# Kernel optimization log

Measured on AMD Instinct MI355X. Metric: run time of the kernel, lower is better.

Reference implementation:

```python
import jax, jax.numpy as jnp
import numpy as np

NUM_SENT, SENT_LEN, HIDDEN, OUT = 128, 64, 512, 512
N = NUM_SENT * SENT_LEN


def setup_inputs() -> dict:
    key = jax.random.key(0)
    ks = jax.random.split(key, 14)
    s = 1.0 / np.sqrt(HIDDEN)
    so = 1.0 / np.sqrt(OUT)
    return {
        "x": jax.random.normal(ks[0], (NUM_SENT, SENT_LEN, HIDDEN), jnp.float32),
        "mask": jax.random.uniform(ks[1], (N,), jnp.float32),
        "a_ud": jax.random.normal(ks[2], (N, N), jnp.float32) * 0.01,
        "a_lr": jax.random.normal(ks[3], (N, N), jnp.float32) * 0.01,
        "W": jax.random.uniform(ks[4], (OUT, HIDDEN), jnp.float32, -s, s),
        "b": jax.random.uniform(ks[5], (OUT,), jnp.float32, -s, s),
        "W_ud": jax.random.uniform(ks[6], (OUT, HIDDEN), jnp.float32, -s, s),
        "b_ud": jax.random.uniform(ks[7], (OUT,), jnp.float32, -s, s),
        "W_lr": jax.random.uniform(ks[8], (OUT, HIDDEN), jnp.float32, -s, s),
        "b_lr": jax.random.uniform(ks[9], (OUT,), jnp.float32, -s, s),
        "W_g": jax.random.uniform(ks[10], (OUT, HIDDEN), jnp.float32, -s, s),
        "b_g": jax.random.uniform(ks[11], (OUT,), jnp.float32, -s, s),
        "W_go": jax.random.uniform(ks[12], (OUT, OUT), jnp.float32, -so, so),
        "b_go": jax.random.uniform(ks[13], (OUT,), jnp.float32, -so, so),
    }


def reference(x, mask, a_ud, a_lr, W, b, W_ud, b_ud, W_lr, b_lr, W_g, b_g, W_go, b_go):
    num_sent, sent_len, hidden = x.shape
    xf = x.reshape(-1, hidden)                       # [N, H]
    h_ud = a_ud @ xf                                 # [N, H] neighbor aggregation (up/down)
    h_lr = a_lr @ xf                                 # [N, H] neighbor aggregation (left/right)
    h = (xf @ W.T + b) + (h_ud @ W_ud.T + b_ud) + (h_lr @ W_lr.T + b_lr)  # [N, OUT]
    # global node branch: masked mean-pool of relu(linear_g(x))
    n = mask.sum()
    h_g = (mask[None, :] @ jax.nn.relu(xf @ W_g.T + b_g)) / n  # [1, OUT]
    h = h + (h_g @ W_go.T + b_go)                    # broadcast add over N rows
    h = jax.nn.relu(h).reshape(num_sent, sent_len, -1)
    return (h, h_g)
```

## Files before the change

kernel.cpp:

```cpp
#include <hip/hip_runtime.h>
#include <stdint.h>


typedef __attribute__((ext_vector_type(8))) short short8;
typedef __attribute__((ext_vector_type(4))) float f32x4;

typedef const __attribute__((address_space(1))) void* gas1_t;
typedef __attribute__((address_space(3))) void* las3_t;

__device__ __forceinline__ void gload16(const void* g, void* l) {
  __builtin_amdgcn_global_load_lds((gas1_t)g, (las3_t)l, 16, 0, 0);
}

__device__ __forceinline__ unsigned pack2t(float lo, float hi) {
  return __builtin_amdgcn_perm(__float_as_uint(hi), __float_as_uint(lo), 0x07060302u);
}

__device__ __forceinline__ unsigned f2bf_rne(float f) {
  unsigned u = __float_as_uint(f);
  return (u + 0x7FFFu + ((u >> 16) & 1u)) >> 16;
}
__device__ __forceinline__ unsigned pack2_rne(float lo, float hi) {
  return f2bf_rne(lo) | (f2bf_rne(hi) << 16);
}

__global__ __launch_bounds__(256) void k1_convert(
    const float* __restrict__ x, const float* __restrict__ W,
    const float* __restrict__ W_ud, const float* __restrict__ W_lr,
    const float* __restrict__ W_g,
    uint16_t* __restrict__ xb, uint16_t* __restrict__ Yt, uint16_t* __restrict__ Wb1)
{
  unsigned tid = blockIdx.x * 256u + threadIdx.x;
  const float* src;
  uint16_t* dst;
  if (tid < 524288u) {
    src = x + (size_t)tid * 8;
    dst = xb + (size_t)tid * 8;
  } else {
    unsigned r = tid - 524288u;
    unsigned which = r >> 15;
    unsigned e8 = (r & 32767u) * 8;
    src = (which == 0 ? W : which == 1 ? W_ud : which == 2 ? W_lr : W_g) + e8;
    if (which == 0) {
      unsigned n = e8 >> 9, k = e8 & 511u;
      dst = Yt + (size_t)n * 16896 + 16384 + k;
    } else {
      dst = Wb1 + (size_t)(which - 1) * 262144 + e8;
    }
  }
  float4 v0 = ((const float4*)src)[0];
  float4 v1 = ((const float4*)src)[1];
  uint4 p;
  p.x = pack2_rne(v0.x, v0.y); p.y = pack2_rne(v0.z, v0.w);
  p.z = pack2_rne(v1.x, v1.y); p.w = pack2_rne(v1.z, v1.w);
  *(uint4*)dst = p;
}

__global__ __launch_bounds__(256) void k2_gemm1(
    const uint16_t* __restrict__ xb, const uint16_t* __restrict__ Wb1,
    const float* __restrict__ mask, const float* __restrict__ b_g,
    uint16_t* __restrict__ Yt, float* __restrict__ tg)
{
  __shared__ __align__(16) char smem[34816];
  char* const bufA = smem;
  char* const bufB = smem + 8192;

  const int t = threadIdx.x;
  const int i0 = blockIdx.x * 128;
  const int bn = blockIdx.y;
  const int n0 = bn * 128;
  const int lane = t & 63, w = t >> 6;
  const int q = lane >> 4, l15 = lane & 15;
  const int wm = w >> 1, wn = w & 1;
  const int srow = t >> 2, spart = t & 3;

  f32x4 acc[4][4] = {};

  const uint16_t* const aA0 = xb + (size_t)(i0 + srow) * 512 + spart * 8;
  const uint16_t* const aA1 = aA0 + (size_t)64 * 512;
  const uint16_t* const aB0 = Wb1 + (size_t)(n0 + srow) * 512 + spart * 8;
  const uint16_t* const aB1 = aB0 + (size_t)64 * 512;

  for (int s = 0; s < 16; ++s) {
    __syncthreads();
    const int kk = s << 5;
    gload16(aA0 + kk, bufA + t * 16);
    gload16(aA1 + kk, bufA + 4096 + t * 16);
    gload16(aB0 + kk, bufB + t * 16);
    gload16(aB1 + kk, bufB + 4096 + t * 16);
    __syncthreads();
    short8 af[4], bf[4];
#pragma unroll
    for (int mi = 0; mi < 4; ++mi)
      af[mi] = *(const short8*)(bufA + (wm * 64 + mi * 16 + l15) * 64 + q * 16);
#pragma unroll
    for (int ni = 0; ni < 4; ++ni)
      bf[ni] = *(const short8*)(bufB + (wn * 64 + ni * 16 + l15) * 64 + q * 16);
#pragma unroll
    for (int mi = 0; mi < 4; ++mi)
#pragma unroll
      for (int ni = 0; ni < 4; ++ni)
        acc[mi][ni] = __builtin_amdgcn_mfma_f32_16x16x32_bf16(af[mi], bf[ni], acc[mi][ni], 0, 0, 0);
  }
  __syncthreads();

  const int g = bn >> 2;
  const int jb = (bn & 3) * 128;

  if (g < 2) {
    uint16_t* T = (uint16_t*)smem;
#pragma unroll
    for (int mi = 0; mi < 4; ++mi) {
#pragma unroll
      for (int ni = 0; ni < 4; ++ni) {
        int jl = wn * 64 + ni * 16 + l15;
#pragma unroll
        for (int r = 0; r < 4; ++r) {
          int il = wm * 64 + mi * 16 + q * 4 + r;
          T[jl * 136 + il] = (uint16_t)f2bf_rne(acc[mi][ni][r]);
        }
      }
    }
    __syncthreads();
    const int jl = t >> 1, half = t & 1;
    uint16_t* dst = Yt + (size_t)(jb + jl) * 16896 + (size_t)g * 8192 + i0 + half * 64;
    const uint16_t* srcT = T + jl * 136 + half * 64;
#pragma unroll
    for (int c = 0; c < 8; ++c)
      *(uint4*)(dst + c * 8) = *(const uint4*)(srcT + c * 8);
  } else {
#pragma unroll
    for (int mi = 0; mi < 4; ++mi) {
#pragma unroll
      for (int ni = 0; ni < 4; ++ni) {
        int jl = jb + wn * 64 + ni * 16 + l15;
        float bg = b_g[jl];
#pragma unroll
        for (int r = 0; r < 4; ++r) {
          int il = i0 + wm * 64 + mi * 16 + q * 4 + r;
          float v = fmaxf(acc[mi][ni][r] + bg, 0.f) * mask[il];
          tg[(size_t)il * 512 + jl] = v;
        }
      }
    }
  }
}

__global__ __launch_bounds__(256) void k3_reduce(const float* __restrict__ tg,
                                                 float* __restrict__ colsum)
{
  const int t = threadIdx.x;
  const int r0 = blockIdx.x * 64;
  float a0 = 0.f, a1 = 0.f;
  for (int r = 0; r < 64; ++r) {
    const float* row = tg + (size_t)(r0 + r) * 512;
    a0 += row[t];
    a1 += row[t + 256];
  }
  atomicAdd(&colsum[t], a0);
  atomicAdd(&colsum[t + 256], a1);
}

__global__ __launch_bounds__(256) void k4_finalize(
    const float* __restrict__ colsum, const float* __restrict__ mask,
    const float* __restrict__ b, const float* __restrict__ b_ud,
    const float* __restrict__ b_lr, const float* __restrict__ W_go,
    const float* __restrict__ b_go,
    float* __restrict__ row_add, float* __restrict__ out_hg)
{
  __shared__ float red[256];
  __shared__ float hg[512];
  const int t = threadIdx.x;
  float s = 0.f;
  for (int k = t; k < 8192; k += 256) s += mask[k];
  red[t] = s;
  __syncthreads();
  for (int o = 128; o > 0; o >>= 1) {
    if (t < o) red[t] += red[t + o];
    __syncthreads();
  }
  const float n = red[0];
  for (int j = t; j < 512; j += 256) hg[j] = colsum[j] / n;
  __syncthreads();

  const int j0 = blockIdx.x * 64;
  const int jj = j0 + (t >> 2);
  const int seg = t & 3;
  const float4* wrow = (const float4*)(W_go + (size_t)jj * 512 + seg * 128);
  float p = 0.f;
#pragma unroll 4
  for (int c = 0; c < 32; ++c) {
    float4 wv = wrow[c];
    const float* h4 = &hg[seg * 128 + c * 4];
    p += wv.x * h4[0] + wv.y * h4[1] + wv.z * h4[2] + wv.w * h4[3];
  }
  p += __shfl_down(p, 2);
  p += __shfl_down(p, 1);
  if ((t & 3) == 0)
    row_add[jj] = b[jj] + b_ud[jj] + b_lr[jj] + b_go[jj] + p;
  if (t < 64) out_hg[j0 + t] = hg[j0 + t];
}

__global__ __launch_bounds__(256) void k5_gemm_big(
    const float* __restrict__ a_ud, const float* __restrict__ a_lr,
    const float* __restrict__ x, const uint16_t* __restrict__ Yt,
    const float* __restrict__ row_add, float* __restrict__ out)
{
  __shared__ __align__(16) char smem[26624];
  char* const bufA0 = smem;
  char* const bufA1 = smem + 5120;
  char* const bufB0 = smem + 10240;
  char* const bufB1 = smem + 18432;

  const int t = threadIdx.x;
  const int i0 = blockIdx.x * 64;
  const int j0 = blockIdx.y * 128;
  const int lane = t & 63, w = t >> 6;
  const int q = lane >> 4, l15 = lane & 15;
  const int wm = w >> 1, wn = w & 1;
  const int srow = t >> 2, spart = t & 3;

  f32x4 acc[2][4] = {};

  const size_t aoff_big = (size_t)(i0 + srow) * 8192 + spart * 8;
  const size_t aoff_x   = (size_t)(i0 + srow) * 512 + spart * 8;
  const uint16_t* const bsrc0 = Yt + (size_t)(j0 + srow) * 16896 + spart * 8;
  const uint16_t* const bsrc1 = bsrc0 + (size_t)64 * 16896;
  const int aw = srow * 80 + spart * 16;

  float4 pA0, pA1;

  {
    const float* asrc = a_ud + aoff_big;
    pA0 = ((const float4*)asrc)[0];
    pA1 = ((const float4*)asrc)[1];
    gload16(bsrc0, bufB0 + t * 16);
    gload16(bsrc1, bufB0 + 4096 + t * 16);
    uint4 pk;
    pk.x = pack2t(pA0.x, pA0.y); pk.y = pack2t(pA0.z, pA0.w);
    pk.z = pack2t(pA1.x, pA1.y); pk.w = pack2t(pA1.z, pA1.w);
    *(uint4*)(bufA0 + aw) = pk;
  }

  for (int s = 0; s < 528; ++s) {
    __syncthreads();
    const int nxt = s + 1;
    const bool more = (nxt < 528);
    char* const cA = (s & 1) ? bufA1 : bufA0;
    char* const cB = (s & 1) ? bufB1 : bufB0;
    char* const nA = (s & 1) ? bufA0 : bufA1;
    char* const nB = (s & 1) ? bufB0 : bufB1;

    if (more) {
      const float* asrc;
      if (nxt < 256)      asrc = a_ud + aoff_big + (nxt << 5);
      else if (nxt < 512) asrc = a_lr + aoff_big + ((nxt - 256) << 5);
      else                asrc = x + aoff_x + ((nxt - 512) << 5);
      pA0 = ((const float4*)asrc)[0];
      pA1 = ((const float4*)asrc)[1];
      const int bk = nxt << 5;
      gload16(bsrc0 + bk, nB + t * 16);
      gload16(bsrc1 + bk, nB + 4096 + t * 16);
    }

    short8 af0 = *(const short8*)(cA + (wm * 32 + l15) * 80 + q * 16);
    short8 af1 = *(const short8*)(cA + (wm * 32 + 16 + l15) * 80 + q * 16);
    short8 bf0 = *(const short8*)(cB + (wn * 64 + l15) * 64 + q * 16);
    short8 bf1 = *(const short8*)(cB + (wn * 64 + 16 + l15) * 64 + q * 16);
    short8 bf2 = *(const short8*)(cB + (wn * 64 + 32 + l15) * 64 + q * 16);
    short8 bf3 = *(const short8*)(cB + (wn * 64 + 48 + l15) * 64 + q * 16);

    acc[0][0] = __builtin_amdgcn_mfma_f32_16x16x32_bf16(af0, bf0, acc[0][0], 0, 0, 0);
    acc[0][1] = __builtin_amdgcn_mfma_f32_16x16x32_bf16(af0, bf1, acc[0][1], 0, 0, 0);
    acc[0][2] = __builtin_amdgcn_mfma_f32_16x16x32_bf16(af0, bf2, acc[0][2], 0, 0, 0);
    acc[0][3] = __builtin_amdgcn_mfma_f32_16x16x32_bf16(af0, bf3, acc[0][3], 0, 0, 0);
    acc[1][0] = __builtin_amdgcn_mfma_f32_16x16x32_bf16(af1, bf0, acc[1][0], 0, 0, 0);
    acc[1][1] = __builtin_amdgcn_mfma_f32_16x16x32_bf16(af1, bf1, acc[1][1], 0, 0, 0);
    acc[1][2] = __builtin_amdgcn_mfma_f32_16x16x32_bf16(af1, bf2, acc[1][2], 0, 0, 0);
    acc[1][3] = __builtin_amdgcn_mfma_f32_16x16x32_bf16(af1, bf3, acc[1][3], 0, 0, 0);

    if (more) {
      uint4 pk;
      pk.x = pack2t(pA0.x, pA0.y); pk.y = pack2t(pA0.z, pA0.w);
      pk.z = pack2t(pA1.x, pA1.y); pk.w = pack2t(pA1.z, pA1.w);
      *(uint4*)(nA + aw) = pk;
    }
  }

#pragma unroll
  for (int ni = 0; ni < 4; ++ni) {
    const int jl = j0 + wn * 64 + ni * 16 + l15;
    const float ra = row_add[jl];
#pragma unroll
    for (int mi = 0; mi < 2; ++mi) {
#pragma unroll
      for (int r = 0; r < 4; ++r) {
        const int il = i0 + wm * 32 + mi * 16 + q * 4 + r;
        out[(size_t)il * 512 + jl] = fmaxf(acc[mi][ni][r] + ra, 0.f);
      }
    }
  }
}

extern "C" void kernel_launch(void* const* d_in, const int* in_sizes, int n_in,
                              void* d_out, int out_size, void* d_ws, size_t ws_size,
                              hipStream_t stream) {
  (void)in_sizes; (void)n_in; (void)out_size; (void)ws_size;
  const float* x    = (const float*)d_in[0];
  const float* mask = (const float*)d_in[1];
  const float* a_ud = (const float*)d_in[2];
  const float* a_lr = (const float*)d_in[3];
  const float* W    = (const float*)d_in[4];
  const float* b    = (const float*)d_in[5];
  const float* W_ud = (const float*)d_in[6];
  const float* b_ud = (const float*)d_in[7];
  const float* W_lr = (const float*)d_in[8];
  const float* b_lr = (const float*)d_in[9];
  const float* W_g  = (const float*)d_in[10];
  const float* b_g  = (const float*)d_in[11];
  const float* W_go = (const float*)d_in[12];
  const float* b_go = (const float*)d_in[13];
  float* out = (float*)d_out;

  char* ws = (char*)d_ws;
  uint16_t* xb     = (uint16_t*)(ws);
  uint16_t* Yt     = (uint16_t*)(ws + 8388608);
  uint16_t* Wb1    = (uint16_t*)(ws + 25690112);
  float*    tg     = (float*)(ws + 27262976);
  float*    colsum = (float*)(ws + 44040192);
  float*    rowadd = (float*)(ws + 44042240);

  hipMemsetAsync(colsum, 0, 512 * sizeof(float), stream);
  k1_convert<<<2560, 256, 0, stream>>>(x, W, W_ud, W_lr, W_g, xb, Yt, Wb1);
  k2_gemm1<<<dim3(64, 12), 256, 0, stream>>>(xb, Wb1, mask, b_g, Yt, tg);
  k3_reduce<<<128, 256, 0, stream>>>(tg, colsum);
  k4_finalize<<<8, 256, 0, stream>>>(colsum, mask, b, b_ud, b_lr, W_go, b_go,
                                     rowadd, out + 4194304);
  k5_gemm_big<<<dim3(128, 4), 256, 0, stream>>>(a_ud, a_lr, x, Yt, rowadd, out);
}
```

Baseline: 1.006 ms.

## Split-K the big GEMM, widen K tile with swizzled LDS, fuse global-pool reduction

The large GEMM now splits its K dimension (a_ud|a_lr|x, 16896) into two halves across blockIdx.z. That doubles the grid from 512 to 1024 blocks to fill more CUs. It also uses a 64-wide K step with an XOR-swizzled B layout in LDS to cut bank conflicts and halve the barrier count. A new combine kernel adds the partial sums, the row bias and applies ReLU, which costs an extra pass over the 16 MB output. The masked relu column sum is folded into the first GEMM epilogue with shuffles and atomics, removing the tg intermediate and the separate reduce kernel.

```diff
diff --git a/kernel.cpp b/kernel.cpp
--- a/kernel.cpp
+++ b/kernel.cpp
@@ -59,7 +59,7 @@
 __global__ __launch_bounds__(256) void k2_gemm1(
     const uint16_t* __restrict__ xb, const uint16_t* __restrict__ Wb1,
     const float* __restrict__ mask, const float* __restrict__ b_g,
-    uint16_t* __restrict__ Yt, float* __restrict__ tg)
+    uint16_t* __restrict__ Yt, float* __restrict__ colsum)
 {
   __shared__ __align__(16) char smem[34816];
   char* const bufA = smem;
@@ -129,36 +129,27 @@
     for (int c = 0; c < 8; ++c)
       *(uint4*)(dst + c * 8) = *(const uint4*)(srcT + c * 8);
   } else {
-#pragma unroll
-    for (int mi = 0; mi < 4; ++mi) {
-#pragma unroll
-      for (int ni = 0; ni < 4; ++ni) {
-        int jl = jb + wn * 64 + ni * 16 + l15;
-        float bg = b_g[jl];
-#pragma unroll
-        for (int r = 0; r < 4; ++r) {
-          int il = i0 + wm * 64 + mi * 16 + q * 4 + r;
-          float v = fmaxf(acc[mi][ni][r] + bg, 0.f) * mask[il];
-          tg[(size_t)il * 512 + jl] = v;
-        }
-      }
-    }
-  }
-}
-
-__global__ __launch_bounds__(256) void k3_reduce(const float* __restrict__ tg,
-                                                 float* __restrict__ colsum)
-{
-  const int t = threadIdx.x;
-  const int r0 = blockIdx.x * 64;
-  float a0 = 0.f, a1 = 0.f;
-  for (int r = 0; r < 64; ++r) {
-    const float* row = tg + (size_t)(r0 + r) * 512;
-    a0 += row[t];
-    a1 += row[t + 256];
-  }
-  atomicAdd(&colsum[t], a0);
-  atomicAdd(&colsum[t + 256], a1);
+    float mk[4][4];
+#pragma unroll
+    for (int mi = 0; mi < 4; ++mi)
+#pragma unroll
+      for (int r = 0; r < 4; ++r)
+        mk[mi][r] = mask[i0 + wm * 64 + mi * 16 + q * 4 + r];
+#pragma unroll
+    for (int ni = 0; ni < 4; ++ni) {
+      const int jl = jb + wn * 64 + ni * 16 + l15;
+      const float bg = b_g[jl];
+      float p = 0.f;
+#pragma unroll
+      for (int mi = 0; mi < 4; ++mi)
+#pragma unroll
+        for (int r = 0; r < 4; ++r)
+          p += fmaxf(acc[mi][ni][r] + bg, 0.f) * mk[mi][r];
+      p += __shfl_xor(p, 16);
+      p += __shfl_xor(p, 32);
+      if (q == 0) atomicAdd(&colsum[jl], p);
+    }
+  }
 }
 
 __global__ __launch_bounds__(256) void k4_finalize(
@@ -204,102 +195,136 @@
 __global__ __launch_bounds__(256) void k5_gemm_big(
     const float* __restrict__ a_ud, const float* __restrict__ a_lr,
     const float* __restrict__ x, const uint16_t* __restrict__ Yt,
-    const float* __restrict__ row_add, float* __restrict__ out)
-{
-  __shared__ __align__(16) char smem[26624];
-  char* const bufA0 = smem;
-  char* const bufA1 = smem + 5120;
-  char* const bufB0 = smem + 10240;
-  char* const bufB1 = smem + 18432;
+    float* __restrict__ out, float* __restrict__ P1)
+{
+  __shared__ __align__(16) char smem[51200];
+  char* const A0 = smem;
+  char* const A1 = smem + 9216;
+  char* const B0 = smem + 18432;
+  char* const B1 = smem + 34816;
 
   const int t = threadIdx.x;
   const int i0 = blockIdx.x * 64;
   const int j0 = blockIdx.y * 128;
-  const int lane = t & 63, w = t >> 6;
+  const int z  = blockIdx.z;
+  const int lane = t & 63;
   const int q = lane >> 4, l15 = lane & 15;
+  const int w = t >> 6;
   const int wm = w >> 1, wn = w & 1;
-  const int srow = t >> 2, spart = t & 3;
+
+  const int arow = t >> 2, aseg = t & 3;
+  const int brow = t >> 3;
+  const int bchunk = (t & 7) ^ ((t >> 3) & 7);
 
   f32x4 acc[2][4] = {};
-
-  const size_t aoff_big = (size_t)(i0 + srow) * 8192 + spart * 8;
-  const size_t aoff_x   = (size_t)(i0 + srow) * 512 + spart * 8;
-  const uint16_t* const bsrc0 = Yt + (size_t)(j0 + srow) * 16896 + spart * 8;
-  const uint16_t* const bsrc1 = bsrc0 + (size_t)64 * 16896;
-  const int aw = srow * 80 + spart * 16;
-
-  float4 pA0, pA1;
+  const int kbase0 = z * 8448;
+
+  float4 av0, av1, av2, av3;
+#define A_SRC(gk) ((gk) < 8192 \
+    ? a_ud + (size_t)(i0 + arow) * 8192 + (gk) + aseg * 16 \
+    : ((gk) < 16384 \
+      ? a_lr + (size_t)(i0 + arow) * 8192 + ((gk) - 8192) + aseg * 16 \
+      : x + (size_t)(i0 + arow) * 512 + ((gk) - 16384) + aseg * 16))
 
   {
-    const float* asrc = a_ud + aoff_big;
-    pA0 = ((const float4*)asrc)[0];
-    pA1 = ((const float4*)asrc)[1];
-    gload16(bsrc0, bufB0 + t * 16);
-    gload16(bsrc1, bufB0 + 4096 + t * 16);
-    uint4 pk;
-    pk.x = pack2t(pA0.x, pA0.y); pk.y = pack2t(pA0.z, pA0.w);
-    pk.z = pack2t(pA1.x, pA1.y); pk.w = pack2t(pA1.z, pA1.w);
-    *(uint4*)(bufA0 + aw) = pk;
-  }
-
-  for (int s = 0; s < 528; ++s) {
-    __syncthreads();
-    const int nxt = s + 1;
-    const bool more = (nxt < 528);
-    char* const cA = (s & 1) ? bufA1 : bufA0;
-    char* const cB = (s & 1) ? bufB1 : bufB0;
-    char* const nA = (s & 1) ? bufA0 : bufA1;
-    char* const nB = (s & 1) ? bufB0 : bufB1;
+    const float* as = A_SRC(kbase0);
+    av0 = ((const float4*)as)[0]; av1 = ((const float4*)as)[1];
+    av2 = ((const float4*)as)[2]; av3 = ((const float4*)as)[3];
+#pragma unroll
+    for (int r = 0; r < 4; ++r) {
+      const int jrow = r * 32 + brow;
+      gload16(Yt + (size_t)(j0 + jrow) * 16896 + kbase0 + bchunk * 8,
+              B0 + r * 4096 + t * 16);
+    }
+    uint4 p0, p1;
+    p0.x = pack2t(av0.x, av0.y); p0.y = pack2t(av0.z, av0.w);
+    p0.z = pack2t(av1.x, av1.y); p0.w = pack2t(av1.z, av1.w);
+    p1.x = pack2t(av2.x, av2.y); p1.y = pack2t(av2.z, av2.w);
+    p1.z = pack2t(av3.x, av3.y); p1.w = pack2t(av3.z, av3.w);
+    *(uint4*)(A0 + arow * 144 + aseg * 32) = p0;
+    *(uint4*)(A0 + arow * 144 + aseg * 32 + 16) = p1;
+  }
+
+  for (int s = 0; s < 132; ++s) {
+    __syncthreads();
+    const bool more = (s + 1 < 132);
+    char* const cA = (s & 1) ? A1 : A0;
+    char* const cB = (s & 1) ? B1 : B0;
+    char* const nA = (s & 1) ? A0 : A1;
+    char* const nB = (s & 1) ? B0 : B1;
 
     if (more) {
-      const float* asrc;
-      if (nxt < 256)      asrc = a_ud + aoff_big + (nxt << 5);
-      else if (nxt < 512) asrc = a_lr + aoff_big + ((nxt - 256) << 5);
-      else                asrc = x + aoff_x + ((nxt - 512) << 5);
-      pA0 = ((const float4*)asrc)[0];
-      pA1 = ((const float4*)asrc)[1];
-      const int bk = nxt << 5;
-      gload16(bsrc0 + bk, nB + t * 16);
-      gload16(bsrc1 + bk, nB + 4096 + t * 16);
-    }
-
-    short8 af0 = *(const short8*)(cA + (wm * 32 + l15) * 80 + q * 16);
-    short8 af1 = *(const short8*)(cA + (wm * 32 + 16 + l15) * 80 + q * 16);
-    short8 bf0 = *(const short8*)(cB + (wn * 64 + l15) * 64 + q * 16);
-    short8 bf1 = *(const short8*)(cB + (wn * 64 + 16 + l15) * 64 + q * 16);
-    short8 bf2 = *(const short8*)(cB + (wn * 64 + 32 + l15) * 64 + q * 16);
-    short8 bf3 = *(const short8*)(cB + (wn * 64 + 48 + l15) * 64 + q * 16);
-
-    acc[0][0] = __builtin_amdgcn_mfma_f32_16x16x32_bf16(af0, bf0, acc[0][0], 0, 0, 0);
-    acc[0][1] = __builtin_amdgcn_mfma_f32_16x16x32_bf16(af0, bf1, acc[0][1], 0, 0, 0);
-    acc[0][2] = __builtin_amdgcn_mfma_f32_16x16x32_bf16(af0, bf2, acc[0][2], 0, 0, 0);
-    acc[0][3] = __builtin_amdgcn_mfma_f32_16x16x32_bf16(af0, bf3, acc[0][3], 0, 0, 0);
-    acc[1][0] = __builtin_amdgcn_mfma_f32_16x16x32_bf16(af1, bf0, acc[1][0], 0, 0, 0);
-    acc[1][1] = __builtin_amdgcn_mfma_f32_16x16x32_bf16(af1, bf1, acc[1][1], 0, 0, 0);
-    acc[1][2] = __builtin_amdgcn_mfma_f32_16x16x32_bf16(af1, bf2, acc[1][2], 0, 0, 0);
-    acc[1][3] = __builtin_amdgcn_mfma_f32_16x16x32_bf16(af1, bf3, acc[1][3], 0, 0, 0);
+      const int gk = kbase0 + (s + 1) * 64;
+      const float* as = A_SRC(gk);
+      av0 = ((const float4*)as)[0]; av1 = ((const float4*)as)[1];
+      av2 = ((const float4*)as)[2]; av3 = ((const float4*)as)[3];
+#pragma unroll
+      for (int r = 0; r < 4; ++r) {
+        const int jrow = r * 32 + brow;
+        gload16(Yt + (size_t)(j0 + jrow) * 16896 + gk + bchunk * 8,
+                nB + r * 4096 + t * 16);
+      }
+    }
+
+#pragma unroll
+    for (int u = 0; u < 2; ++u) {
+      const int c = u * 4 + q;
+      const int r0 = wm * 32 + l15;
+      short8 af0 = *(const short8*)(cA + r0 * 144 + c * 16);
+      short8 af1 = *(const short8*)(cA + (r0 + 16) * 144 + c * 16);
+      short8 bfr[4];
+#pragma unroll
+      for (int ni = 0; ni < 4; ++ni) {
+        const int jbr = wn * 64 + ni * 16 + l15;
+        bfr[ni] = *(const short8*)(cB + jbr * 128 + (c ^ (jbr & 7)) * 16);
+      }
+#pragma unroll
+      for (int ni = 0; ni < 4; ++ni) {
+        acc[0][ni] = __builtin_amdgcn_mfma_f32_16x16x32_bf16(af0, bfr[ni], acc[0][ni], 0, 0, 0);
+        acc[1][ni] = __builtin_amdgcn_mfma_f32_16x16x32_bf16(af1, bfr[ni], acc[1][ni], 0, 0, 0);
+      }
+    }
 
     if (more) {
-      uint4 pk;
-      pk.x = pack2t(pA0.x, pA0.y); pk.y = pack2t(pA0.z, pA0.w);
-      pk.z = pack2t(pA1.x, pA1.y); pk.w = pack2t(pA1.z, pA1.w);
-      *(uint4*)(nA + aw) = pk;
-    }
-  }
-
+      uint4 p0, p1;
+      p0.x = pack2t(av0.x, av0.y); p0.y = pack2t(av0.z, av0.w);
+      p0.z = pack2t(av1.x, av1.y); p0.w = pack2t(av1.z, av1.w);
+      p1.x = pack2t(av2.x, av2.y); p1.y = pack2t(av2.z, av2.w);
+      p1.z = pack2t(av3.x, av3.y); p1.w = pack2t(av3.z, av3.w);
+      *(uint4*)(nA + arow * 144 + aseg * 32) = p0;
+      *(uint4*)(nA + arow * 144 + aseg * 32 + 16) = p1;
+    }
+  }
+#undef A_SRC
+
+  float* dst = z ? P1 : out;
 #pragma unroll
   for (int ni = 0; ni < 4; ++ni) {
     const int jl = j0 + wn * 64 + ni * 16 + l15;
-    const float ra = row_add[jl];
-#pragma unroll
-    for (int mi = 0; mi < 2; ++mi) {
+#pragma unroll
+    for (int mi = 0; mi < 2; ++mi)
 #pragma unroll
       for (int r = 0; r < 4; ++r) {
         const int il = i0 + wm * 32 + mi * 16 + q * 4 + r;
-        out[(size_t)il * 512 + jl] = fmaxf(acc[mi][ni][r] + ra, 0.f);
-      }
-    }
-  }
+        dst[(size_t)il * 512 + jl] = acc[mi][ni][r];
+      }
+  }
+}
+
+__global__ __launch_bounds__(256) void k6_combine(
+    const float* __restrict__ P1, const float* __restrict__ row_add,
+    float* __restrict__ out)
+{
+  const int idx = blockIdx.x * 256 + threadIdx.x;
+  const float4 a = ((const float4*)out)[idx];
+  const float4 p = ((const float4*)P1)[idx];
+  const float4 r = ((const float4*)row_add)[idx & 127];
+  float4 o;
+  o.x = fmaxf(a.x + p.x + r.x, 0.f);
+  o.y = fmaxf(a.y + p.y + r.y, 0.f);
+  o.z = fmaxf(a.z + p.z + r.z, 0.f);
+  o.w = fmaxf(a.w + p.w + r.w, 0.f);
+  ((float4*)out)[idx] = o;
 }
 
 extern "C" void kernel_launch(void* const* d_in, const int* in_sizes, int n_in,
@@ -326,15 +351,15 @@
   uint16_t* xb     = (uint16_t*)(ws);
   uint16_t* Yt     = (uint16_t*)(ws + 8388608);
   uint16_t* Wb1    = (uint16_t*)(ws + 25690112);
-  float*    tg     = (float*)(ws + 27262976);
-  float*    colsum = (float*)(ws + 44040192);
-  float*    rowadd = (float*)(ws + 44042240);
+  float*    colsum = (float*)(ws + 27262976);
+  float*    rowadd = (float*)(ws + 27265024);
+  float*    P1     = (float*)(ws + 27267072);
 
   hipMemsetAsync(colsum, 0, 512 * sizeof(float), stream);
   k1_convert<<<2560, 256, 0, stream>>>(x, W, W_ud, W_lr, W_g, xb, Yt, Wb1);
-  k2_gemm1<<<dim3(64, 12), 256, 0, stream>>>(xb, Wb1, mask, b_g, Yt, tg);
-  k3_reduce<<<128, 256, 0, stream>>>(tg, colsum);
+  k2_gemm1<<<dim3(64, 12), 256, 0, stream>>>(xb, Wb1, mask, b_g, Yt, colsum);
   k4_finalize<<<8, 256, 0, stream>>>(colsum, mask, b, b_ud, b_lr, W_go, b_go,
                                      rowadd, out + 4194304);
-  k5_gemm_big<<<dim3(128, 4), 256, 0, stream>>>(a_ud, a_lr, x, Yt, rowadd, out);
-}
+  k5_gemm_big<<<dim3(128, 4, 2), 256, 0, stream>>>(a_ud, a_lr, x, Yt, out, P1);
+  k6_combine<<<4096, 256, 0, stream>>>(P1, rowadd, out);
+}
```

Measured after the change: 902.0 us. 10.3% less time.
